# Kernel tuning notes

Measured on AMD Instinct MI355X. Metric: run time of the kernel, lower is better.

## Reference

```python
import jax, jax.numpy as jnp
import numpy as np

NEG = -1e9  # stands in for -inf in masked_fill; identical softmax output, grad-safe


def _sfu(inputs, fusion, Wr, Wg):
    # SFU: m = [x, f, x*f, x-f]; o = relu(m@Wr)*g + (1-g)*x, g = sigmoid(m@Wg)
    m = jnp.concatenate([inputs, fusion, inputs * fusion, inputs - fusion], axis=-1)
    x = jax.nn.relu(m @ Wr)
    g = jax.nn.sigmoid(m @ Wg)
    return x * g + (1.0 - g) * inputs


def _stage(U, V, cmask, qmask, E, B, p):
    # One Aligner stage = InterAlign followed by SelfAlign. Batch-first layout (b, len, d).
    Wu, bu, Wv, bv, Wri, Wgi, gi, W1, b1, W2, b2, Wrs, Wgs, gs = p
    # ---- InterAlign ----
    Ct = jax.nn.relu(U @ Wu + bu)              # (b, c, d)
    Qt = jax.nn.relu(V @ Wv + bv)              # (b, q, d)
    E0 = jnp.einsum('bcd,bqd->bcq', Ct, Qt)    # (b, c, q)
    if E is not None:
        Es = jax.nn.softmax(jnp.where(cmask[:, :, None] == 0, NEG, E), axis=1)   # softmax over c
        Bs = jax.nn.softmax(jnp.where(cmask[:, None, :] == 0, NEG, B), axis=2)   # softmax over c (cols)
        E = E0 + gi * jnp.einsum('bce,beq->bcq', Bs, Es)
    else:
        E = E0
    Ett = jax.nn.softmax(jnp.where(qmask[:, None, :] == 0, NEG, E), axis=2)
    qctx = jnp.einsum('bcq,bqd->bcd', Ett, V)  # attend question
    h = _sfu(U, qctx, Wri, Wgi)
    # ---- SelfAlign ----
    H1 = jax.nn.relu(h @ W1 + b1)
    H2 = jax.nn.relu(h @ W2 + b2)
    B0 = jnp.einsum('bcd,bed->bce', H1, H2)    # (b, c, c)
    if B is not None:
        B1s = jax.nn.softmax(jnp.where(cmask[:, :, None] == 0, NEG, B), axis=1)
        B2s = jax.nn.softmax(jnp.where(cmask[:, None, :] == 0, NEG, B), axis=2)
        B = B0 + gs * jnp.einsum('bce,bef->bcf', B2s, B1s)
    else:
        B = B0
    c = U.shape[1]
    B = B * (1.0 - jnp.eye(c, dtype=B.dtype))[None]  # masked_fill_(eye, 0.0): zero diagonal
    Btt = jax.nn.softmax(jnp.where(cmask[:, None, :] == 0, NEG, B), axis=2)
    hctx = jnp.einsum('bce,bed->bcd', Btt, h)
    Z = _sfu(h, hctx, Wrs, Wgs)
    return Z, E, B


def setup_inputs() -> dict:
    key = jax.random.key(0)
    b, c_len, q_len, d = 8, 768, 96, 768
    T = 2  # number of aligner stages
    ks = jax.random.split(key, 16)
    s = 0.02
    inp = {
        'U': jax.random.normal(ks[0], (b, c_len, d), jnp.float32),
        'V': jax.random.normal(ks[1], (b, q_len, d), jnp.float32),
        'U_mask': jax.random.randint(ks[2], (b, c_len), 0, 2).astype(jnp.int32),
        'V_mask': jax.random.randint(ks[3], (b, q_len), 0, 2).astype(jnp.int32),
        'Wu': jax.random.normal(ks[4], (T, d, d), jnp.float32) * s,
        'bu': jnp.zeros((T, d), jnp.float32),
        'Wv': jax.random.normal(ks[5], (T, d, d), jnp.float32) * s,
        'bv': jnp.zeros((T, d), jnp.float32),
        'Wr_i': jax.random.normal(ks[6], (T, 4 * d, d), jnp.float32) * s,
        'Wg_i': jax.random.normal(ks[7], (T, 4 * d, d), jnp.float32) * s,
        'gamma_i': jnp.full((T,), 3.0, jnp.float32),
        'W1': jax.random.normal(ks[8], (T, d, d), jnp.float32) * s,
        'b1': jnp.zeros((T, d), jnp.float32),
        'W2': jax.random.normal(ks[9], (T, d, d), jnp.float32) * s,
        'b2': jnp.zeros((T, d), jnp.float32),
        'Wr_s': jax.random.normal(ks[10], (T, 4 * d, d), jnp.float32) * s,
        'Wg_s': jax.random.normal(ks[11], (T, 4 * d, d), jnp.float32) * s,
        'gamma_s': jnp.full((T,), 3.0, jnp.float32),
    }
    return inp


def reference(U, V, U_mask, V_mask, Wu, bu, Wv, bv, Wr_i, Wg_i, gamma_i,
              W1, b1, W2, b2, Wr_s, Wg_s, gamma_s):
    E = None
    B = None
    x = U
    for t in range(Wu.shape[0]):  # fixed small stage loop (align_1 -> align_2)
        p = (Wu[t], bu[t], Wv[t], bv[t], Wr_i[t], Wg_i[t], gamma_i[t],
             W1[t], b1[t], W2[t], b2[t], Wr_s[t], Wg_s[t], gamma_s[t])
        x, E, B = _stage(x, V, U_mask, V_mask, E, B, p)
    return x
```

## Files before the change

kernel.cpp:

```cpp
#include <hip/hip_runtime.h>
#include <math.h>

#define NEGV -1e9f

typedef short bf16x8 __attribute__((ext_vector_type(8)));
typedef float f32x4 __attribute__((ext_vector_type(4)));
typedef unsigned short ushort8v __attribute__((ext_vector_type(8)));

static __device__ __forceinline__ unsigned short f2bf(float f) {
  unsigned int u = __float_as_uint(f);
  unsigned int r = (u + 0x7fffu + ((u >> 16) & 1u)) >> 16;
  return (unsigned short)r;
}

static __device__ __forceinline__ int xcd_swz(int lin, int nwg) {
  int q = nwg >> 3, r = nwg & 7;
  int x = lin & 7, i = lin >> 3;
  return (x < r) ? x * (q + 1) + i : r * (q + 1) + (x - r) * q + i;
}

__device__ __forceinline__ float wred_max(float v) {
  #pragma unroll
  for (int o = 32; o > 0; o >>= 1) v = fmaxf(v, __shfl_down(v, o, 64));
  return v;
}
__device__ __forceinline__ float wred_sum(float v) {
  #pragma unroll
  for (int o = 32; o > 0; o >>= 1) v += __shfl_down(v, o, 64);
  return v;
}

__global__ __launch_bounds__(256)
void softmax_row_mask(const float* __restrict__ X, const int* __restrict__ mask,
                      float* __restrict__ Y, unsigned short* __restrict__ Ybf,
                      int R, int Cn)
{
  int bz = blockIdx.y, r = blockIdx.x, tid = threadIdx.x;
  const float* xr = X + ((size_t)bz * R + r) * Cn;
  const int*   mr = mask + (size_t)bz * Cn;
  float*       yr = Y ? (Y + ((size_t)bz * R + r) * Cn) : nullptr;
  unsigned short* yb = Ybf ? (Ybf + ((size_t)bz * R + r) * Cn) : nullptr;
  __shared__ float sred[4], sred2[4];

  float m = -INFINITY, s = 0.f;
  for (int i = tid; i < Cn; i += 256) {
    float v = (mr[i] != 0) ? xr[i] : NEGV;
    float nm = fmaxf(m, v);
    s = s * expf(m - nm) + expf(v - nm);
    m = nm;
  }
  float wm = wred_max(m);
  if ((tid & 63) == 0) sred[tid >> 6] = wm;
  __syncthreads();
  float fm = fmaxf(fmaxf(sred[0], sred[1]), fmaxf(sred[2], sred[3]));
  float sadj = s * expf(m - fm);
  float wsv = wred_sum(sadj);
  if ((tid & 63) == 0) sred2[tid >> 6] = wsv;
  __syncthreads();
  float fs = sred2[0] + sred2[1] + sred2[2] + sred2[3];
  float inv = 1.0f / fs;

  for (int i = tid; i < Cn; i += 256) {
    float v = (mr[i] != 0) ? xr[i] : NEGV;
    float o = expf(v - fm) * inv;
    if (yr) yr[i] = o;
    if (yb) yb[i] = f2bf(o);
  }
}

__global__ __launch_bounds__(256)
void colsoftmax_T(const float* __restrict__ X, const int* __restrict__ mask,
                  unsigned short* __restrict__ Y, int n)
{
  int bz = blockIdx.y;
  const float* Xb = X + (size_t)bz * n * n;
  const int*   mr = mask + (size_t)bz * n;
  unsigned short* Yb = Y + (size_t)bz * n * n;
  __shared__ float T[64][65];
  __shared__ float rm[4][64], rs[4][64];
  __shared__ float sm[64], sinv[64];
  int j0 = blockIdx.x * 64;
  int t = threadIdx.x;
  int tr = t >> 4, tc4 = (t & 15) * 4;
  int jj = t & 63, qq = t >> 6;
  const int NTile = n / 64;

  float m = -INFINITY, s = 0.f;
  for (int it = 0; it < NTile; ++it) {
    int i0 = it * 64;
    __syncthreads();
    #pragma unroll
    for (int r = 0; r < 4; ++r) {
      int i = tr + r * 16;
      float4 v = *reinterpret_cast<const float4*>(Xb + (size_t)(i0 + i) * n + j0 + tc4);
      int mk = mr[i0 + i];
      T[i][tc4 + 0] = mk ? v.x : NEGV;
      T[i][tc4 + 1] = mk ? v.y : NEGV;
      T[i][tc4 + 2] = mk ? v.z : NEGV;
      T[i][tc4 + 3] = mk ? v.w : NEGV;
    }
    __syncthreads();
    #pragma unroll
    for (int r = 0; r < 16; ++r) {
      float v = T[qq * 16 + r][jj];
      float nm = fmaxf(m, v);
      s = s * expf(m - nm) + expf(v - nm);
      m = nm;
    }
  }
  rm[qq][jj] = m; rs[qq][jj] = s;
  __syncthreads();
  if (t < 64) {
    float m0 = rm[0][t], m1 = rm[1][t], m2 = rm[2][t], m3 = rm[3][t];
    float fm = fmaxf(fmaxf(m0, m1), fmaxf(m2, m3));
    float fs = rs[0][t] * expf(m0 - fm) + rs[1][t] * expf(m1 - fm)
             + rs[2][t] * expf(m2 - fm) + rs[3][t] * expf(m3 - fm);
    sm[t] = fm; sinv[t] = 1.0f / fs;
  }
  __syncthreads();

  for (int it = 0; it < NTile; ++it) {
    int i0 = it * 64;
    __syncthreads();
    #pragma unroll
    for (int r = 0; r < 4; ++r) {
      int i = tr + r * 16;
      float4 v = *reinterpret_cast<const float4*>(Xb + (size_t)(i0 + i) * n + j0 + tc4);
      int mk = mr[i0 + i];
      T[i][tc4 + 0] = mk ? v.x : NEGV;
      T[i][tc4 + 1] = mk ? v.y : NEGV;
      T[i][tc4 + 2] = mk ? v.z : NEGV;
      T[i][tc4 + 3] = mk ? v.w : NEGV;
    }
    __syncthreads();
    #pragma unroll
    for (int r = 0; r < 4; ++r) {
      int jr = tr + r * 16;
      float fm = sm[jr], inv = sinv[jr];
      ushort4 o;
      o.x = f2bf(expf(T[tc4 + 0][jr] - fm) * inv);
      o.y = f2bf(expf(T[tc4 + 1][jr] - fm) * inv);
      o.z = f2bf(expf(T[tc4 + 2][jr] - fm) * inv);
      o.w = f2bf(expf(T[tc4 + 3][jr] - fm) * inv);
      *reinterpret_cast<ushort4*>(Yb + (size_t)(j0 + jr) * n + i0 + tc4) = o;
    }
  }
}

__global__ __launch_bounds__(256)
void transp_f32(const float* __restrict__ X, float* __restrict__ Y,
                int R, int C, long sX, long sY)
{
  int bz = blockIdx.z;
  X += (size_t)bz * sX;
  Y += (size_t)bz * sY;
  __shared__ float T[64][65];
  int c0 = blockIdx.x * 64, r0 = blockIdx.y * 64;
  int t = threadIdx.x;
  int tr = t >> 4, tc4 = (t & 15) * 4;
  #pragma unroll
  for (int rr = 0; rr < 4; ++rr) {
    int r = tr + rr * 16;
    float4 v = make_float4(0.f, 0.f, 0.f, 0.f);
    if (c0 + tc4 < C)
      v = *reinterpret_cast<const float4*>(X + (size_t)(r0 + r) * C + c0 + tc4);
    T[r][tc4 + 0] = v.x; T[r][tc4 + 1] = v.y;
    T[r][tc4 + 2] = v.z; T[r][tc4 + 3] = v.w;
  }
  __syncthreads();
  #pragma unroll
  for (int rr = 0; rr < 4; ++rr) {
    int cc = tr + rr * 16;
    int gc = c0 + cc;
    if (gc < C) {
      float4 o = make_float4(T[tc4 + 0][cc], T[tc4 + 1][cc], T[tc4 + 2][cc], T[tc4 + 3][cc]);
      *reinterpret_cast<float4*>(Y + (size_t)gc * R + r0 + tc4) = o;
    }
  }
}

__global__ __launch_bounds__(256)
void transpV(const float* __restrict__ V, unsigned short* __restrict__ VT)
{
  int bz = blockIdx.z;
  const float* Vb = V + (size_t)bz * 96 * 768;
  unsigned short* Yb = VT + (size_t)bz * 768 * 96;
  __shared__ float T[64][65];
  int c0 = blockIdx.x * 64, r0 = blockIdx.y * 64;
  int t = threadIdx.x;
  int tr = t >> 4, tc4 = (t & 15) * 4;
  #pragma unroll
  for (int rr = 0; rr < 4; ++rr) {
    int r = tr + rr * 16;
    int gr = r0 + r;
    float4 v = make_float4(0.f, 0.f, 0.f, 0.f);
    if (gr < 96)
      v = *reinterpret_cast<const float4*>(Vb + (size_t)gr * 768 + c0 + tc4);
    T[r][tc4 + 0] = v.x; T[r][tc4 + 1] = v.y;
    T[r][tc4 + 2] = v.z; T[r][tc4 + 3] = v.w;
  }
  __syncthreads();
  #pragma unroll
  for (int rr = 0; rr < 4; ++rr) {
    int cc = tr + rr * 16;
    int gc = c0 + cc;
    #pragma unroll
    for (int e = 0; e < 4; ++e) {
      int gr = r0 + tc4 + e;
      if (gr < 96) Yb[(size_t)gc * 96 + gr] = f2bf(T[tc4 + e][cc]);
    }
  }
}

__global__ __launch_bounds__(256)
void concat_bf16(const float* __restrict__ X, const float* __restrict__ F,
                 unsigned short* __restrict__ Mc)
{
  int idx = blockIdx.x * 256 + threadIdx.x;
  int m  = idx / 96;
  int kk = (idx - m * 96) * 8;
  const float* xp = X + (size_t)m * 768 + kk;
  const float* fp = F + (size_t)m * 768 + kk;
  float4 a0 = *reinterpret_cast<const float4*>(xp);
  float4 a1 = *reinterpret_cast<const float4*>(xp + 4);
  float4 b0 = *reinterpret_cast<const float4*>(fp);
  float4 b1 = *reinterpret_cast<const float4*>(fp + 4);
  float xa[8] = {a0.x, a0.y, a0.z, a0.w, a1.x, a1.y, a1.z, a1.w};
  float fa[8] = {b0.x, b0.y, b0.z, b0.w, b1.x, b1.y, b1.z, b1.w};
  ushort8v o0, o1, o2;
  #pragma unroll
  for (int i = 0; i < 8; ++i) {
    o0[i] = f2bf(xa[i]);
    o1[i] = f2bf(fa[i]);
    o2[i] = f2bf(xa[i] * fa[i]);
  }
  unsigned short* base = Mc + (size_t)m * 2304 + kk;
  *reinterpret_cast<ushort8v*>(base)        = o0;
  *reinterpret_cast<ushort8v*>(base +  768) = o1;
  *reinterpret_cast<ushort8v*>(base + 1536) = o2;
}

__global__ __launch_bounds__(256)
void transp_cast4(const float* __restrict__ W0, const float* __restrict__ W1a,
                  const float* __restrict__ W2a, const float* __restrict__ W3a,
                  unsigned short* __restrict__ Wt)
{
  int z = blockIdx.z;
  const float* W = (z == 0) ? W0 : (z == 1) ? W1a : (z == 2) ? W2a : W3a;
  unsigned short* Y = Wt + (size_t)z * 768 * 768;
  __shared__ float T[64][65];
  int n0 = blockIdx.x * 64, k0 = blockIdx.y * 64;
  int t = threadIdx.x;
  int tr = t >> 4, tc4 = (t & 15) * 4;
  #pragma unroll
  for (int r = 0; r < 4; ++r) {
    int k = tr + r * 16;
    float4 v = *reinterpret_cast<const float4*>(W + (size_t)(k0 + k) * 768 + n0 + tc4);
    T[k][tc4 + 0] = v.x; T[k][tc4 + 1] = v.y; T[k][tc4 + 2] = v.z; T[k][tc4 + 3] = v.w;
  }
  __syncthreads();
  #pragma unroll
  for (int r = 0; r < 4; ++r) {
    int n = tr + r * 16;
    ushort4 o;
    o.x = f2bf(T[tc4 + 0][n]); o.y = f2bf(T[tc4 + 1][n]);
    o.z = f2bf(T[tc4 + 2][n]); o.w = f2bf(T[tc4 + 3][n]);
    *reinterpret_cast<ushort4*>(Y + (size_t)(n0 + n) * 768 + k0 + tc4) = o;
  }
}

__global__ __launch_bounds__(256)
void transp_cast2(const float* __restrict__ Wa, const float* __restrict__ Wb,
                  unsigned short* __restrict__ Wt)
{
  const float* W = blockIdx.z ? Wb : Wa;
  unsigned short* Y = Wt + (size_t)blockIdx.z * 768 * 2304;
  __shared__ float T[64][65];
  int n0 = blockIdx.x * 64, k0 = blockIdx.y * 64;
  int t = threadIdx.x;
  int tr = t >> 4, tc4 = (t & 15) * 4;
  #pragma unroll
  for (int r = 0; r < 4; ++r) {
    int k = tr + r * 16;
    int gk = k0 + k;
    float4 v = *reinterpret_cast<const float4*>(W + (size_t)gk * 768 + n0 + tc4);
    if (gk < 768) {
      float4 u = *reinterpret_cast<const float4*>(W + (size_t)(gk + 2304) * 768 + n0 + tc4);
      v.x += u.x; v.y += u.y; v.z += u.z; v.w += u.w;
    } else if (gk < 1536) {
      float4 u = *reinterpret_cast<const float4*>(W + (size_t)(gk + 1536) * 768 + n0 + tc4);
      v.x -= u.x; v.y -= u.y; v.z -= u.z; v.w -= u.w;
    }
    T[k][tc4 + 0] = v.x; T[k][tc4 + 1] = v.y; T[k][tc4 + 2] = v.z; T[k][tc4 + 3] = v.w;
  }
  __syncthreads();
  #pragma unroll
  for (int r = 0; r < 4; ++r) {
    int n = tr + r * 16;
    ushort4 o;
    o.x = f2bf(T[tc4 + 0][n]); o.y = f2bf(T[tc4 + 1][n]);
    o.z = f2bf(T[tc4 + 2][n]); o.w = f2bf(T[tc4 + 3][n]);
    *reinterpret_cast<ushort4*>(Y + (size_t)(n0 + n) * 2304 + k0 + tc4) = o;
  }
}

__global__ __launch_bounds__(256)
void transp_cast(const float* __restrict__ W, unsigned short* __restrict__ Wt,
                 int K, long sW, long sWt)
{
  int bz = blockIdx.z;
  W  += (size_t)bz * sW;
  Wt += (size_t)bz * sWt;
  __shared__ float T[64][65];
  int n0 = blockIdx.x * 64, k0 = blockIdx.y * 64;
  int t = threadIdx.x;
  int tr = t >> 4, tc4 = (t & 15) * 4;
  #pragma unroll
  for (int r = 0; r < 4; ++r) {
    int k = tr + r * 16;
    float4 v = *reinterpret_cast<const float4*>(W + (size_t)(k0 + k) * 768 + n0 + tc4);
    T[k][tc4 + 0] = v.x; T[k][tc4 + 1] = v.y; T[k][tc4 + 2] = v.z; T[k][tc4 + 3] = v.w;
  }
  __syncthreads();
  #pragma unroll
  for (int r = 0; r < 4; ++r) {
    int n = tr + r * 16;
    ushort4 o;
    o.x = f2bf(T[tc4 + 0][n]); o.y = f2bf(T[tc4 + 1][n]);
    o.z = f2bf(T[tc4 + 2][n]); o.w = f2bf(T[tc4 + 3][n]);
    *reinterpret_cast<ushort4*>(Wt + (size_t)(n0 + n) * K + k0 + tc4) = o;
  }
}

__global__ __launch_bounds__(256)
void cast_bf16(const float* __restrict__ X, unsigned short* __restrict__ Y, int n8)
{
  int idx = blockIdx.x * 256 + threadIdx.x;
  if (idx >= n8) return;
  float4 a0 = *reinterpret_cast<const float4*>(X + (size_t)idx * 8);
  float4 a1 = *reinterpret_cast<const float4*>(X + (size_t)idx * 8 + 4);
  ushort8v o;
  o[0] = f2bf(a0.x); o[1] = f2bf(a0.y); o[2] = f2bf(a0.z); o[3] = f2bf(a0.w);
  o[4] = f2bf(a1.x); o[5] = f2bf(a1.y); o[6] = f2bf(a1.z); o[7] = f2bf(a1.w);
  *reinterpret_cast<ushort8v*>(Y + (size_t)idx * 8) = o;
}


template<int NB, int WAVES>
__global__ __launch_bounds__(64 * WAVES)
void mfma_gemm(const unsigned short* __restrict__ A,
               const unsigned short* __restrict__ Bt0,
               const unsigned short* __restrict__ Bt1,
               const float* __restrict__ bias0, const float* __restrict__ bias1,
               const float* __restrict__ alphap, const float* __restrict__ C0,
               float* __restrict__ F0, float* __restrict__ F1,
               unsigned short* __restrict__ O0, unsigned short* __restrict__ O1,
               int M, int N, int K,
               long sA, long sB, long sC0, long sC,
               int relu, int zerodiag)
{
  const int RG = WAVES / 4;
  const int TM = RG * 48;
  __shared__ unsigned short As[2][TM * 32];
  __shared__ unsigned short Bs0[2][2048];
  __shared__ unsigned short Bs1[2][NB == 2 ? 2048 : 16];

  int nx = gridDim.x, ny = gridDim.y;
  int nwg = nx * ny * gridDim.z;
  int lin = blockIdx.x + nx * (blockIdx.y + ny * blockIdx.z);
  int sw = xcd_swz(lin, nwg);
  int bxi = sw % nx; int rest = sw / nx;
  int byi = rest % ny; int bz = rest / ny;

  A   += (size_t)bz * sA;
  Bt0 += (size_t)bz * sB;
  if (NB == 2) Bt1 += (size_t)bz * sB;
  const float* C0b = C0 ? (C0 + (size_t)bz * sC0) : nullptr;

  int tid = threadIdx.x;
  int w = tid >> 6, l = tid & 63;
  int m0 = byi * TM, n0 = bxi * 64;
  int wr = w >> 2, wc = w & 3;

  int g8 = (((l & 3) ^ ((l >> 3) & 3))) * 8;
  int rowA = w * 16 + (l >> 2); if (rowA > TM - 1) rowA = TM - 1;
  int rB = n0 + (w & 3) * 16 + (l >> 2); if (rB > N - 1) rB = N - 1;
  const unsigned short* srcA  = A + (size_t)(m0 + rowA) * K + g8;
  const unsigned short* srcB0 = Bt0 + (size_t)rB * K + g8;
  const unsigned short* srcB1 = (NB == 2) ? Bt1 + (size_t)rB * K + g8 : nullptr;

#define GG_STAGE(kt, bi) do { int kk0 = (kt) * 32;                                                                        \
    if (w < TM / 16)                                                                                                      \
      __builtin_amdgcn_global_load_lds((const unsigned int*)(srcA + kk0),  (unsigned int*)&As[bi][0]  + w * 256, 16, 0, 0); \
    if (w < 4)                                                                                                            \
      __builtin_amdgcn_global_load_lds((const unsigned int*)(srcB0 + kk0), (unsigned int*)&Bs0[bi][0] + w * 256, 16, 0, 0); \
    if (NB == 2 && w >= 4)                                                                                                \
      __builtin_amdgcn_global_load_lds((const unsigned int*)(srcB1 + kk0), (unsigned int*)&Bs1[bi][0] + (w - 4) * 256, 16, 0, 0); \
  } while (0)

  f32x4 a0[3] = {};
  f32x4 a1v[3] = {};

  const int NT = K / 32;
  int prm = ((l >> 4) ^ ((l >> 1) & 3)) * 8;
  GG_STAGE(0, 0);
  __syncthreads();
  int cur = 0;
  for (int kt = 0; kt < NT; ++kt) {
    if (kt + 1 < NT) GG_STAGE(kt + 1, cur ^ 1);

    bf16x8 af[3];
    #pragma unroll
    for (int i = 0; i < 3; ++i) {
      int off = (wr * 48 + i * 16 + (l & 15)) * 32 + prm;
      af[i] = *reinterpret_cast<const bf16x8*>(&As[cur][off]);
    }
    int offB = (wc * 16 + (l & 15)) * 32 + prm;
    bf16x8 b0 = *reinterpret_cast<const bf16x8*>(&Bs0[cur][offB]);
    #pragma unroll
    for (int i = 0; i < 3; ++i)
      a0[i] = __builtin_amdgcn_mfma_f32_16x16x32_bf16(af[i], b0, a0[i], 0, 0, 0);
    if (NB == 2) {
      bf16x8 b1 = *reinterpret_cast<const bf16x8*>(&Bs1[cur][offB]);
      #pragma unroll
      for (int i = 0; i < 3; ++i)
        a1v[i] = __builtin_amdgcn_mfma_f32_16x16x32_bf16(af[i], b1, a1v[i], 0, 0, 0);
    }
    __syncthreads();
    cur ^= 1;
  }
#undef GG_STAGE

  float alpha = alphap ? alphap[0] : 1.0f;
  float* F0b = F0 ? F0 + (size_t)bz * sC : nullptr;
  float* F1b = F1 ? F1 + (size_t)bz * sC : nullptr;
  unsigned short* O0b = O0 ? O0 + (size_t)bz * sC : nullptr;
  unsigned short* O1b = O1 ? O1 + (size_t)bz * sC : nullptr;

  #pragma unroll
  for (int i = 0; i < 3; ++i) {
    #pragma unroll
    for (int qq = 0; qq < 4; ++qq) {
      int gm = m0 + wr * 48 + i * 16 + (l >> 4) * 4 + qq;
      int gn = n0 + wc * 16 + (l & 15);
      if (gn >= N) continue;
      size_t oidx = (size_t)gm * N + gn;
      float v = alpha * a0[i][qq];
      if (bias0) v += bias0[gn];
      if (relu) v = fmaxf(v, 0.f);
      if (C0b) v += C0b[oidx];
      if (zerodiag && gm == gn) v = 0.f;
      if (F0b) F0b[oidx] = v;
      if (O0b) O0b[oidx] = f2bf(v);
      if (NB == 2) {
        float v1 = alpha * a1v[i][qq];
        if (bias1) v1 += bias1[gn];
        if (relu) v1 = fmaxf(v1, 0.f);
        if (F1b) F1b[oidx] = v1;
        if (O1b) O1b[oidx] = f2bf(v1);
      }
    }
  }
}

__global__ __launch_bounds__(512)
void sfu_mfma(const unsigned short* __restrict__ Mc,
              const unsigned short* __restrict__ Brt,
              const unsigned short* __restrict__ Bgt,
              const float* __restrict__ Xres, float* __restrict__ Z,
              unsigned short* __restrict__ Zb)
{
  __shared__ unsigned short As[2][3072];
  __shared__ unsigned short Brs[2][2048];
  __shared__ unsigned short Bgs[2][2048];
  const int K = 2304;
  const int NT = 72;

  int nx = gridDim.x, ny = gridDim.y;
  int nwg = nx * ny;
  int lin = blockIdx.x + nx * blockIdx.y;
  int sw = xcd_swz(lin, nwg);
  int bxi = sw % nx; int byi = sw / nx;

  int tid = threadIdx.x;
  int w = tid >> 6, l = tid & 63;
  int m0 = byi * 96, n0 = bxi * 64;
  int wr = w >> 2, wc = w & 3;

  int g8 = (((l & 3) ^ ((l >> 3) & 3))) * 8;
  int rowA = w * 16 + (l >> 2); if (rowA > 95) rowA = 95;
  int rB = n0 + (w & 3) * 16 + (l >> 2);
  const unsigned short* srcA = Mc  + (size_t)(m0 + rowA) * K + g8;
  const unsigned short* srcR = Brt + (size_t)rB * K + g8;
  const unsigned short* srcG = Bgt + (size_t)rB * K + g8;

#define SFU_STAGE(kt, bi) do { int kk0 = (kt) * 32;                                                                      \
    if (w < 6)                                                                                                           \
      __builtin_amdgcn_global_load_lds((const unsigned int*)(srcA + kk0), (unsigned int*)&As[bi][0]  + w * 256, 16, 0, 0); \
    if (w < 4)                                                                                                           \
      __builtin_amdgcn_global_load_lds((const unsigned int*)(srcR + kk0), (unsigned int*)&Brs[bi][0] + w * 256, 16, 0, 0); \
    if (w >= 4)                                                                                                          \
      __builtin_amdgcn_global_load_lds((const unsigned int*)(srcG + kk0), (unsigned int*)&Bgs[bi][0] + (w - 4) * 256, 16, 0, 0); \
  } while (0)

  f32x4 aR[3] = {};
  f32x4 aG[3] = {};

  int prm = ((l >> 4) ^ ((l >> 1) & 3)) * 8;
  SFU_STAGE(0, 0);
  __syncthreads();
  int cur = 0;
  for (int kt = 0; kt < NT; ++kt) {
    if (kt + 1 < NT) SFU_STAGE(kt + 1, cur ^ 1);

    bf16x8 af[3];
    #pragma unroll
    for (int i = 0; i < 3; ++i) {
      int off = (wr * 48 + i * 16 + (l & 15)) * 32 + prm;
      af[i] = *reinterpret_cast<const bf16x8*>(&As[cur][off]);
    }
    int offB = (wc * 16 + (l & 15)) * 32 + prm;
    bf16x8 br = *reinterpret_cast<const bf16x8*>(&Brs[cur][offB]);
    bf16x8 bg = *reinterpret_cast<const bf16x8*>(&Bgs[cur][offB]);
    #pragma unroll
    for (int i = 0; i < 3; ++i) {
      aR[i] = __builtin_amdgcn_mfma_f32_16x16x32_bf16(af[i], br, aR[i], 0, 0, 0);
      aG[i] = __builtin_amdgcn_mfma_f32_16x16x32_bf16(af[i], bg, aG[i], 0, 0, 0);
    }
    __syncthreads();
    cur ^= 1;
  }
#undef SFU_STAGE

  #pragma unroll
  for (int i = 0; i < 3; ++i) {
    #pragma unroll
    for (int qq = 0; qq < 4; ++qq) {
      int gm = m0 + wr * 48 + i * 16 + (l >> 4) * 4 + qq;
      int gn = n0 + wc * 16 + (l & 15);
      float r = fmaxf(aR[i][qq], 0.f);
      float g = 1.0f / (1.0f + expf(-aG[i][qq]));
      float xv = Xres[(size_t)gm * 768 + gn];
      float z = r * g + (1.0f - g) * xv;
      Z[(size_t)gm * 768 + gn] = z;
      if (Zb) Zb[(size_t)gm * 768 + gn] = f2bf(z);
    }
  }
}

static void launch_mfma1(const unsigned short* A, const unsigned short* Bt,
                         const float* bias, const float* alphap, const float* C0,
                         float* F0, unsigned short* O0,
                         int M, int N, int K, long sA, long sB, long sC0, long sC,
                         int relu, int zd, int batch, int tm, hipStream_t s)
{
  dim3 g((N + 63) / 64, M / tm, batch);
  if (tm == 48)
    mfma_gemm<1, 4><<<g, 256, 0, s>>>(A, Bt, nullptr, bias, nullptr, alphap, C0,
                                      F0, nullptr, O0, nullptr, M, N, K, sA, sB, sC0, sC, relu, zd);
  else
    mfma_gemm<1, 8><<<g, 512, 0, s>>>(A, Bt, nullptr, bias, nullptr, alphap, C0,
                                      F0, nullptr, O0, nullptr, M, N, K, sA, sB, sC0, sC, relu, zd);
}

static void launch_mfma2(const unsigned short* A, const unsigned short* Bt0,
                         const unsigned short* Bt1, const float* bias0, const float* bias1,
                         unsigned short* O0, unsigned short* O1,
                         int M, int N, int K, long sA, long sB,
                         int relu, int batch, hipStream_t s)
{
  dim3 g((N + 63) / 64, M / 96, batch);
  mfma_gemm<2, 8><<<g, 512, 0, s>>>(A, Bt0, Bt1, bias0, bias1, nullptr, nullptr,
                                    nullptr, nullptr, O0, O1, M, N, K, sA, sB, 0, sA,
                                    relu, 0);
}

static void launch_sfu(const float* x, const float* f, const float* Wr, const float* Wg,
                       const float* xres, float* z, unsigned short* zb,
                       unsigned short* Mc, unsigned short* Wt, hipStream_t s)
{
  concat_bf16<<<dim3(2304), 256, 0, s>>>(x, f, Mc);
  unsigned short* Wrt = Wt;
  unsigned short* Wgt = Wt + (size_t)768 * 2304;
  transp_cast2<<<dim3(12, 36, 2), 256, 0, s>>>(Wr, Wg, Wt);
  sfu_mfma<<<dim3(12, 64), 512, 0, s>>>(Mc, Wrt, Wgt, xres, z, zb);
}

extern "C" void kernel_launch(void* const* d_in, const int* in_sizes, int n_in,
                              void* d_out, int out_size, void* d_ws, size_t ws_size,
                              hipStream_t stream)
{
  const int b = 8, c = 768, q = 96, d = 768, T = 2;
  const float* U   = (const float*)d_in[0];
  const float* V   = (const float*)d_in[1];
  const int*   Um  = (const int*)d_in[2];
  const int*   Vm  = (const int*)d_in[3];
  const float* Wu  = (const float*)d_in[4];
  const float* bu  = (const float*)d_in[5];
  const float* Wv  = (const float*)d_in[6];
  const float* bv  = (const float*)d_in[7];
  const float* Wri = (const float*)d_in[8];
  const float* Wgi = (const float*)d_in[9];
  const float* gi  = (const float*)d_in[10];
  const float* W1  = (const float*)d_in[11];
  const float* b1  = (const float*)d_in[12];
  const float* W2  = (const float*)d_in[13];
  const float* b2  = (const float*)d_in[14];
  const float* Wrs = (const float*)d_in[15];
  const float* Wgs = (const float*)d_in[16];
  const float* gs  = (const float*)d_in[17];
  float* out = (float*)d_out;

  const size_t big = (size_t)b * c * d;
  const size_t smE = (size_t)b * c * q;
  float* ws   = (float*)d_ws;
  float* xbuf = ws + 0 * big;
  float* h    = ws + 1 * big;
  float* Bm   = ws + 2 * big;
  float* t1   = ws + 3 * big;
  float* t2   = ws + 4 * big;
  float* t3   = ws + 5 * big;
  float* t4   = ws + 6 * big;
  float* Ebuf = ws + 7 * big;
  float* E0b  = Ebuf + smE;
  float* Esb  = E0b + smE;
  float* spare = Esb + smE;
  float* slotE = spare + smE;
  float* WTf  = slotE + big / 2;

  unsigned short* Mc  = (unsigned short*)t1;
  unsigned short* Wt  = (unsigned short*)t4;
  unsigned short* t1h = (unsigned short*)t1;
  unsigned short* t3h = (unsigned short*)t3;
  unsigned short* t3h2 = t3h + big;
  unsigned short* slotEb = (unsigned short*)slotE;
  unsigned short* H1b = t1h;
  unsigned short* H2b = H1b + big;
  unsigned short* WuT = (unsigned short*)WTf;
  unsigned short* WvT  = WuT  + (size_t)d * d;
  unsigned short* W1T  = WvT  + (size_t)d * d;
  unsigned short* W2T  = W1T  + (size_t)d * d;
  unsigned short* Vb16 = W2T  + (size_t)d * d;
  unsigned short* Qtbb = Vb16 + smE;
  unsigned short* VTb  = Qtbb + smE;
  unsigned short* EsTb = VTb  + smE;
  unsigned short* Ettb = EsTb + smE;

  const long cd = (long)c * d, cq = (long)c * q, qd = (long)q * d, cc = (long)c * c;
  const size_t dd = (size_t)d * d;
  const int cast_big = (int)(big / 8);
  (void)ws_size; (void)spare;

  const float* x = U;
  for (int t = 0; t < T; ++t) {
    const float* Writ = Wri + (size_t)t * 4 * dd;
    const float* Wgit = Wgi + (size_t)t * 4 * dd;
    const float* Wrst = Wrs + (size_t)t * 4 * dd;
    const float* Wgst = Wgs + (size_t)t * 4 * dd;

    transp_cast4<<<dim3(12, 12, 4), 256, 0, stream>>>(Wu + t * dd, Wv + t * dd,
                                                      W1 + t * dd, W2 + t * dd, WuT);
    if (t == 0) {
      cast_bf16<<<dim3((int)(smE / 8 / 256)), 256, 0, stream>>>(V, Vb16, (int)(smE / 8));
      transpV<<<dim3(12, 2, b), 256, 0, stream>>>(V, VTb);
      cast_bf16<<<dim3(cast_big / 256), 256, 0, stream>>>(x, t3h, cast_big);
    }

    launch_mfma1(t3h, WuT, bu + t * d, nullptr, nullptr, nullptr, t1h,
                 b * c, d, d, 0, 0, 0, 0, 1, 0, 1, 96, stream);
    launch_mfma1(Vb16, WvT, bv + t * d, nullptr, nullptr, nullptr, Qtbb,
                 b * q, d, d, 0, 0, 0, 0, 1, 0, 1, 48, stream);
    float* e0dst = (t == 0) ? Ebuf : E0b;
    launch_mfma1(t1h, Qtbb, nullptr, nullptr, nullptr, e0dst, nullptr,
                 c, q, d, cd, qd, 0, cq, 0, 0, b, 48, stream);
    if (t > 0) {
      transp_f32<<<dim3(2, 12, b), 256, 0, stream>>>(Ebuf, Esb, c, q, cq, cq);
      softmax_row_mask<<<dim3(q, b), 256, 0, stream>>>(Esb, Um, nullptr, EsTb, q, c);
      softmax_row_mask<<<dim3(c, b), 256, 0, stream>>>(Bm, Um, nullptr, slotEb, c, c);
      launch_mfma1(slotEb, EsTb, nullptr, gi + t, E0b, Ebuf, nullptr,
                   c, q, c, cc, cq, cq, cq, 0, 0, b, 48, stream);
    }
    softmax_row_mask<<<dim3(c, b), 256, 0, stream>>>(Ebuf, Vm, nullptr, Ettb, c, q);
    launch_mfma1(Ettb, VTb, nullptr, nullptr, nullptr, t4, nullptr,
                 c, d, q, cq, qd, 0, cd, 0, 0, b, 96, stream);
    launch_sfu(x, t4, Writ, Wgit, x, h, t3h, Mc, Wt, stream);
    launch_mfma2(t3h, W1T, W2T, b1 + t * d, b2 + t * d, H1b, H2b,
                 b * c, d, d, 0, 0, 1, 1, stream);
    if (t == 0) {
      launch_mfma1(H1b, H2b, nullptr, nullptr, nullptr, Bm, nullptr,
                   c, c, d, cd, cd, 0, cc, 0, 1, b, 96, stream);
    } else {
      launch_mfma1(H1b, H2b, nullptr, nullptr, nullptr, xbuf, nullptr,
                   c, c, d, cd, cd, 0, cc, 0, 0, b, 96, stream);
      colsoftmax_T<<<dim3(12, b), 256, 0, stream>>>(Bm, Um, t3h2, c);
      launch_mfma1(slotEb, t3h2, nullptr, gs + t, xbuf, Bm, nullptr,
                   c, c, c, cc, cc, cc, cc, 0, 1, b, 96, stream);
    }
    softmax_row_mask<<<dim3(c, b), 256, 0, stream>>>(Bm, Um, nullptr, t3h2, c, c);
    transp_cast<<<dim3(12, 12, b), 256, 0, stream>>>(h, slotEb, 768, cd, cd);
    launch_mfma1(t3h2, slotEb, nullptr, nullptr, nullptr, t4, nullptr,
                 c, d, c, cc, cd, 0, cd, 0, 0, b, 96, stream);
    float* zdst = (t == T - 1) ? out : xbuf;
    unsigned short* zb16 = (t == T - 1) ? nullptr : t3h;
    launch_sfu(h, t4, Wrst, Wgst, h, zdst, zb16, Mc, Wt, stream);

    x = xbuf;
  }
}
```

Measured before the change: 770.7 us.

## Fuse stage-2 self-align GEMMs and split column softmax into stats/emit

```diff
diff --git a/kernel.cpp b/kernel.cpp
--- a/kernel.cpp
+++ b/kernel.cpp
@@ -40,73 +40,70 @@
   const int*   mr = mask + (size_t)bz * Cn;
   float*       yr = Y ? (Y + ((size_t)bz * R + r) * Cn) : nullptr;
   unsigned short* yb = Ybf ? (Ybf + ((size_t)bz * R + r) * Cn) : nullptr;
-  __shared__ float sred[4], sred2[4];
-
-  float m = -INFINITY, s = 0.f;
+  __shared__ float sred[4];
+
+  float mx = -INFINITY;
   for (int i = tid; i < Cn; i += 256) {
     float v = (mr[i] != 0) ? xr[i] : NEGV;
+    mx = fmaxf(mx, v);
+  }
+  float wm = wred_max(mx);
+  if ((tid & 63) == 0) sred[tid >> 6] = wm;
+  __syncthreads();
+  mx = fmaxf(fmaxf(sred[0], sred[1]), fmaxf(sred[2], sred[3]));
+  __syncthreads();
+
+  float s = 0.f;
+  for (int i = tid; i < Cn; i += 256) {
+    float v = (mr[i] != 0) ? xr[i] : NEGV;
+    s += expf(v - mx);
+  }
+  float wsv = wred_sum(s);
+  if ((tid & 63) == 0) sred[tid >> 6] = wsv;
+  __syncthreads();
+  s = sred[0] + sred[1] + sred[2] + sred[3];
+  float inv = 1.0f / s;
+
+  for (int i = tid; i < Cn; i += 256) {
+    float v = (mr[i] != 0) ? xr[i] : NEGV;
+    float o = expf(v - mx) * inv;
+    if (yr) yr[i] = o;
+    if (yb) yb[i] = f2bf(o);
+  }
+}
+
+__global__ __launch_bounds__(256)
+void colsm_stats(const float* __restrict__ X, const int* __restrict__ mask,
+                 float* __restrict__ SM, float* __restrict__ SS, int n)
+{
+  int bz = blockIdx.z;
+  const float* Xb = X + (size_t)bz * n * n;
+  const int*   mr = mask + (size_t)bz * n;
+  __shared__ float T[64][65];
+  __shared__ float rm[4][64], rs[4][64];
+  int j0 = blockIdx.x * 64, i0 = blockIdx.y * 64;
+  int t = threadIdx.x;
+  int tr = t >> 4, tc4 = (t & 15) * 4;
+  int jj = t & 63, qq = t >> 6;
+
+  #pragma unroll
+  for (int r = 0; r < 4; ++r) {
+    int i = tr + r * 16;
+    float4 v = *reinterpret_cast<const float4*>(Xb + (size_t)(i0 + i) * n + j0 + tc4);
+    int mk = mr[i0 + i];
+    T[i][tc4 + 0] = mk ? v.x : NEGV;
+    T[i][tc4 + 1] = mk ? v.y : NEGV;
+    T[i][tc4 + 2] = mk ? v.z : NEGV;
+    T[i][tc4 + 3] = mk ? v.w : NEGV;
+  }
+  __syncthreads();
+  float m = -INFINITY, s = 0.f;
+  #pragma unroll
+  for (int r = 0; r < 16; ++r) {
+    float v = T[qq * 16 + r][jj];
     float nm = fmaxf(m, v);
     s = s * expf(m - nm) + expf(v - nm);
     m = nm;
-  }
-  float wm = wred_max(m);
-  if ((tid & 63) == 0) sred[tid >> 6] = wm;
-  __syncthreads();
-  float fm = fmaxf(fmaxf(sred[0], sred[1]), fmaxf(sred[2], sred[3]));
-  float sadj = s * expf(m - fm);
-  float wsv = wred_sum(sadj);
-  if ((tid & 63) == 0) sred2[tid >> 6] = wsv;
-  __syncthreads();
-  float fs = sred2[0] + sred2[1] + sred2[2] + sred2[3];
-  float inv = 1.0f / fs;
-
-  for (int i = tid; i < Cn; i += 256) {
-    float v = (mr[i] != 0) ? xr[i] : NEGV;
-    float o = expf(v - fm) * inv;
-    if (yr) yr[i] = o;
-    if (yb) yb[i] = f2bf(o);
-  }
-}
-
-__global__ __launch_bounds__(256)
-void colsoftmax_T(const float* __restrict__ X, const int* __restrict__ mask,
-                  unsigned short* __restrict__ Y, int n)
-{
-  int bz = blockIdx.y;
-  const float* Xb = X + (size_t)bz * n * n;
-  const int*   mr = mask + (size_t)bz * n;
-  unsigned short* Yb = Y + (size_t)bz * n * n;
-  __shared__ float T[64][65];
-  __shared__ float rm[4][64], rs[4][64];
-  __shared__ float sm[64], sinv[64];
-  int j0 = blockIdx.x * 64;
-  int t = threadIdx.x;
-  int tr = t >> 4, tc4 = (t & 15) * 4;
-  int jj = t & 63, qq = t >> 6;
-  const int NTile = n / 64;
-
-  float m = -INFINITY, s = 0.f;
-  for (int it = 0; it < NTile; ++it) {
-    int i0 = it * 64;
-    __syncthreads();
-    #pragma unroll
-    for (int r = 0; r < 4; ++r) {
-      int i = tr + r * 16;
-      float4 v = *reinterpret_cast<const float4*>(Xb + (size_t)(i0 + i) * n + j0 + tc4);
-      int mk = mr[i0 + i];
-      T[i][tc4 + 0] = mk ? v.x : NEGV;
-      T[i][tc4 + 1] = mk ? v.y : NEGV;
-      T[i][tc4 + 2] = mk ? v.z : NEGV;
-      T[i][tc4 + 3] = mk ? v.w : NEGV;
-    }
-    __syncthreads();
-    #pragma unroll
-    for (int r = 0; r < 16; ++r) {
-      float v = T[qq * 16 + r][jj];
-      float nm = fmaxf(m, v);
-      s = s * expf(m - nm) + expf(v - nm);
-      m = nm;
-    }
   }
   rm[qq][jj] = m; rs[qq][jj] = s;
   __syncthreads();
@@ -115,35 +112,57 @@
     float fm = fmaxf(fmaxf(m0, m1), fmaxf(m2, m3));
     float fs = rs[0][t] * expf(m0 - fm) + rs[1][t] * expf(m1 - fm)
              + rs[2][t] * expf(m2 - fm) + rs[3][t] * expf(m3 - fm);
+    size_t base = (((size_t)bz * gridDim.x + blockIdx.x) * gridDim.y + blockIdx.y) * 64 + t;
+    SM[base] = fm; SS[base] = fs;
+  }
+}
+
+__global__ __launch_bounds__(256)
+void colsm_emit(const float* __restrict__ X, const int* __restrict__ mask,
+                const float* __restrict__ SM, const float* __restrict__ SS,
+                unsigned short* __restrict__ Y, int n)
+{
+  int bz = blockIdx.z;
+  const float* Xb = X + (size_t)bz * n * n;
+  const int*   mr = mask + (size_t)bz * n;
+  unsigned short* Yb = Y + (size_t)bz * n * n;
+  __shared__ float T[64][65];
+  __shared__ float sm[64], sinv[64];
+  int j0 = blockIdx.x * 64, i0 = blockIdx.y * 64;
+  int t = threadIdx.x;
+  int tr = t >> 4, tc4 = (t & 15) * 4;
+  int nt = gridDim.y;
+
+  if (t < 64) {
+    size_t base = (((size_t)bz * gridDim.x + blockIdx.x) * nt) * 64 + t;
+    float fm = -INFINITY;
+    for (int it = 0; it < nt; ++it) fm = fmaxf(fm, SM[base + (size_t)it * 64]);
+    float fs = 0.f;
+    for (int it = 0; it < nt; ++it)
+      fs += SS[base + (size_t)it * 64] * expf(SM[base + (size_t)it * 64] - fm);
     sm[t] = fm; sinv[t] = 1.0f / fs;
   }
-  __syncthreads();
-
-  for (int it = 0; it < NTile; ++it) {
-    int i0 = it * 64;
-    __syncthreads();
-    #pragma unroll
-    for (int r = 0; r < 4; ++r) {
-      int i = tr + r * 16;
-      float4 v = *reinterpret_cast<const float4*>(Xb + (size_t)(i0 + i) * n + j0 + tc4);
-      int mk = mr[i0 + i];
-      T[i][tc4 + 0] = mk ? v.x : NEGV;
-      T[i][tc4 + 1] = mk ? v.y : NEGV;
-      T[i][tc4 + 2] = mk ? v.z : NEGV;
-      T[i][tc4 + 3] = mk ? v.w : NEGV;
-    }
-    __syncthreads();
-    #pragma unroll
-    for (int r = 0; r < 4; ++r) {
-      int jr = tr + r * 16;
-      float fm = sm[jr], inv = sinv[jr];
-      ushort4 o;
-      o.x = f2bf(expf(T[tc4 + 0][jr] - fm) * inv);
-      o.y = f2bf(expf(T[tc4 + 1][jr] - fm) * inv);
-      o.z = f2bf(expf(T[tc4 + 2][jr] - fm) * inv);
-      o.w = f2bf(expf(T[tc4 + 3][jr] - fm) * inv);
-      *reinterpret_cast<ushort4*>(Yb + (size_t)(j0 + jr) * n + i0 + tc4) = o;
-    }
+  #pragma unroll
+  for (int r = 0; r < 4; ++r) {
+    int i = tr + r * 16;
+    float4 v = *reinterpret_cast<const float4*>(Xb + (size_t)(i0 + i) * n + j0 + tc4);
+    int mk = mr[i0 + i];
+    T[i][tc4 + 0] = mk ? v.x : NEGV;
+    T[i][tc4 + 1] = mk ? v.y : NEGV;
+    T[i][tc4 + 2] = mk ? v.z : NEGV;
+    T[i][tc4 + 3] = mk ? v.w : NEGV;
+  }
+  __syncthreads();
+  #pragma unroll
+  for (int r = 0; r < 4; ++r) {
+    int jr = tr + r * 16;
+    float fm = sm[jr], inv = sinv[jr];
+    ushort4 o;
+    o.x = f2bf(expf(T[tc4 + 0][jr] - fm) * inv);
+    o.y = f2bf(expf(T[tc4 + 1][jr] - fm) * inv);
+    o.z = f2bf(expf(T[tc4 + 2][jr] - fm) * inv);
+    o.w = f2bf(expf(T[tc4 + 3][jr] - fm) * inv);
+    *reinterpret_cast<ushort4*>(Yb + (size_t)(j0 + jr) * n + i0 + tc4) = o;
   }
 }
 
@@ -459,6 +478,101 @@
         if (F1b) F1b[oidx] = v1;
         if (O1b) O1b[oidx] = f2bf(v1);
       }
+    }
+  }
+}
+
+__global__ __launch_bounds__(512)
+void mfma_dual2(const unsigned short* __restrict__ A1,
+                const unsigned short* __restrict__ B1t,
+                const unsigned short* __restrict__ A2,
+                const unsigned short* __restrict__ B2t,
+                const float* __restrict__ alphap, float* __restrict__ F0,
+                int M, int N, int K,
+                long sA1, long sB1, long sA2, long sB2, long sC,
+                int zerodiag)
+{
+  __shared__ unsigned short As1[2][3072], Bs1[2][2048];
+  __shared__ unsigned short As2[2][3072], Bs2[2][2048];
+
+  int nx = gridDim.x, ny = gridDim.y;
+  int nwg = nx * ny * gridDim.z;
+  int lin = blockIdx.x + nx * (blockIdx.y + ny * blockIdx.z);
+  int sw = xcd_swz(lin, nwg);
+  int bxi = sw % nx; int rest = sw / nx;
+  int byi = rest % ny; int bz = rest / ny;
+
+  A1  += (size_t)bz * sA1;
+  B1t += (size_t)bz * sB1;
+  A2  += (size_t)bz * sA2;
+  B2t += (size_t)bz * sB2;
+
+  int tid = threadIdx.x;
+  int w = tid >> 6, l = tid & 63;
+  int m0 = byi * 96, n0 = bxi * 64;
+  int wr = w >> 2, wc = w & 3;
+
+  int g8 = (((l & 3) ^ ((l >> 3) & 3))) * 8;
+  int rowA = w * 16 + (l >> 2); if (rowA > 95) rowA = 95;
+  int rB = n0 + (w & 3) * 16 + (l >> 2);
+  const unsigned short* srcA1 = A1 + (size_t)(m0 + rowA) * K + g8;
+  const unsigned short* srcA2 = A2 + (size_t)(m0 + rowA) * K + g8;
+  const unsigned short* srcB1 = B1t + (size_t)rB * K + g8;
+  const unsigned short* srcB2 = B2t + (size_t)rB * K + g8;
+
+#define D2_STAGE(kt, bi) do { int kk0 = (kt) * 32;                                                                        \
+    if (w < 6) {                                                                                                          \
+      __builtin_amdgcn_global_load_lds((const unsigned int*)(srcA1 + kk0), (unsigned int*)&As1[bi][0] + w * 256, 16, 0, 0); \
+      __builtin_amdgcn_global_load_lds((const unsigned int*)(srcA2 + kk0), (unsigned int*)&As2[bi][0] + w * 256, 16, 0, 0); \
+    }                                                                                                                     \
+    if (w < 4)                                                                                                            \
+      __builtin_amdgcn_global_load_lds((const unsigned int*)(srcB1 + kk0), (unsigned int*)&Bs1[bi][0] + w * 256, 16, 0, 0); \
+    else                                                                                                                  \
+      __builtin_amdgcn_global_load_lds((const unsigned int*)(srcB2 + kk0), (unsigned int*)&Bs2[bi][0] + (w - 4) * 256, 16, 0, 0); \
+  } while (0)
+
+  f32x4 ac1[3] = {};
+  f32x4 ac2[3] = {};
+
+  const int NT = K / 32;
+  int prm = ((l >> 4) ^ ((l >> 1) & 3)) * 8;
+  D2_STAGE(0, 0);
+  __syncthreads();
+  int cur = 0;
+  for (int kt = 0; kt < NT; ++kt) {
+    if (kt + 1 < NT) D2_STAGE(kt + 1, cur ^ 1);
+
+    int offB = (wc * 16 + (l & 15)) * 32 + prm;
+    bf16x8 af1[3], af2[3];
+    #pragma unroll
+    for (int i = 0; i < 3; ++i) {
+      int off = (wr * 48 + i * 16 + (l & 15)) * 32 + prm;
+      af1[i] = *reinterpret_cast<const bf16x8*>(&As1[cur][off]);
+      af2[i] = *reinterpret_cast<const bf16x8*>(&As2[cur][off]);
+    }
+    bf16x8 b1 = *reinterpret_cast<const bf16x8*>(&Bs1[cur][offB]);
+    bf16x8 b2 = *reinterpret_cast<const bf16x8*>(&Bs2[cur][offB]);
+    #pragma unroll
+    for (int i = 0; i < 3; ++i) {
+      ac1[i] = __builtin_amdgcn_mfma_f32_16x16x32_bf16(af1[i], b1, ac1[i], 0, 0, 0);
+      ac2[i] = __builtin_amdgcn_mfma_f32_16x16x32_bf16(af2[i], b2, ac2[i], 0, 0, 0);
+    }
+    __syncthreads();
+    cur ^= 1;
+  }
+#undef D2_STAGE
+
+  float alpha = alphap[0];
+  float* F0b = F0 + (size_t)bz * sC;
+  #pragma unroll
+  for (int i = 0; i < 3; ++i) {
+    #pragma unroll
+    for (int qq = 0; qq < 4; ++qq) {
+      int gm = m0 + wr * 48 + i * 16 + (l >> 4) * 4 + qq;
+      int gn = n0 + wc * 16 + (l & 15);
+      float v = ac1[i][qq] + alpha * ac2[i][qq];
+      if (zerodiag && gm == gn) v = 0.f;
+      F0b[(size_t)gm * N + gn] = v;
     }
   }
 }
@@ -636,6 +750,8 @@
   unsigned short* slotEb = (unsigned short*)slotE;
   unsigned short* H1b = t1h;
   unsigned short* H2b = H1b + big;
+  float* SMst = spare;
+  float* SSst = spare + 73728;
   unsigned short* WuT = (unsigned short*)WTf;
   unsigned short* WvT  = WuT  + (size_t)d * d;
   unsigned short* W1T  = WvT  + (size_t)d * d;
@@ -649,7 +765,7 @@
   const long cd = (long)c * d, cq = (long)c * q, qd = (long)q * d, cc = (long)c * c;
   const size_t dd = (size_t)d * d;
   const int cast_big = (int)(big / 8);
-  (void)ws_size; (void)spare;
+  (void)ws_size;
 
   const float* x = U;
   for (int t = 0; t < T; ++t) {
@@ -690,11 +806,11 @@
       launch_mfma1(H1b, H2b, nullptr, nullptr, nullptr, Bm, nullptr,
                    c, c, d, cd, cd, 0, cc, 0, 1, b, 96, stream);
     } else {
-      launch_mfma1(H1b, H2b, nullptr, nullptr, nullptr, xbuf, nullptr,
-                   c, c, d, cd, cd, 0, cc, 0, 0, b, 96, stream);
-      colsoftmax_T<<<dim3(12, b), 256, 0, stream>>>(Bm, Um, t3h2, c);
-      launch_mfma1(slotEb, t3h2, nullptr, gs + t, xbuf, Bm, nullptr,
-                   c, c, c, cc, cc, cc, cc, 0, 1, b, 96, stream);
+      colsm_stats<<<dim3(12, 12, b), 256, 0, stream>>>(Bm, Um, SMst, SSst, c);
+      colsm_emit<<<dim3(12, 12, b), 256, 0, stream>>>(Bm, Um, SMst, SSst, t3h2, c);
+      mfma_dual2<<<dim3(12, 8, b), 512, 0, stream>>>(H1b, H2b, slotEb, t3h2,
+                                                     gs + t, Bm,
+                                                     c, c, d, cd, cd, cc, cc, cc, 1);
     }
     softmax_row_mask<<<dim3(c, b), 256, 0, stream>>>(Bm, Um, nullptr, t3h2, c, c);
     transp_cast<<<dim3(12, 12, b), 256, 0, stream>>>(h, slotEb, 768, cd, cd);
```

Result: faster. 733.4 us (-4.8%).
